# Optimization experiments

Measured on AMD Instinct MI355X. Metric: run time of the kernel, lower is better.

The kernel has to match this reference:

```python
import jax, jax.numpy as jnp
import numpy as np

B, T, D_IN = 64, 365, 10
D_MODEL, N_HEAD, D_K = 256, 16, 8
D_HEAD = D_MODEL // N_HEAD  # 16, value head dim
MAX_POS = 365 + 2 * 30      # max_position + 2*max_temporal_shift = 425
BN_EPS = 1e-5


def _pos_table(n_pos, d, temp=1000.0):
    # standard sinusoidal table (frozen in the original via Embedding.from_pretrained)
    pos = np.arange(n_pos)[:, None].astype(np.float64)
    i = np.arange(d)[None, :]
    angle = pos / np.power(temp, 2 * (i // 2) / d)
    tab = np.where(i % 2 == 0, np.sin(angle), np.cos(angle))
    return jnp.asarray(tab, jnp.float32)

POS_TABLE = _pos_table(MAX_POS, D_MODEL)


def _linear_layer(x, W, b, g, beta):
    # LinearLayer = Linear -> BatchNorm1d (train-mode batch stats, per-feature) -> ReLU
    y = x @ W.T + b
    ax = tuple(range(y.ndim - 1))
    mu = y.mean(ax, keepdims=True)
    var = y.var(ax, keepdims=True)  # biased var, matches torch BN
    y = (y - mu) * jax.lax.rsqrt(var + BN_EPS) * g + beta
    return jax.nn.relu(y)


def _forward(positions, x, w1, b1, g1, e1, w2, b2, g2, e2, w3, b3, g3, e3,
             ws1, ws2, wi, bi, gi, ei, wk, bk, wq, bq, wm, bm, gm, em,
             wd1, bd1, gd1, ed1, wd2, bd2, gd2, ed2, wc, bc):
    # channel MLP encoder: 10 -> 64 -> 128 -> 256
    out = _linear_layer(x, w1, b1, g1, e1)
    out = _linear_layer(out, w2, b2, g2, e2)
    out = _linear_layer(out, w3, b3, g3, e3)                    # [B,T,256]
    # channel SE attention: avgpool over time, 2 linears (no bias), sigmoid, residual
    pooled = out.mean(axis=1, keepdims=True)                     # [B,1,256]
    att = jax.nn.sigmoid(jax.nn.relu(pooled @ ws1.T) @ ws2.T)    # [B,1,256]
    out = att * pooled + out                                     # broadcast residual
    # temporal attention block
    h = _linear_layer(out, wi, bi, gi, ei)                       # inconv -> [B,T,256]
    e = h + POS_TABLE[positions]                                 # add positional encoding
    q = (e @ wq.T + bq).reshape(B, T, N_HEAD, D_K)
    k = (e @ wk.T + bk).reshape(B, T, N_HEAD, D_K)
    v = e.reshape(B, T, N_HEAD, D_HEAD)
    # 'cross' attention: full score matrix, mean over key dim, softmax over query dim
    scores = jnp.einsum('bthd,bshd->bhts', q, k) / jnp.sqrt(jnp.float32(D_K))  # [B,H,T,T]
    scores = scores.mean(axis=-1)                                # [B,H,T]
    a = jax.nn.softmax(scores, axis=-1)                          # [B,H,T]
    y = jnp.einsum('bht,bthe->bhe', a, v).reshape(B, D_MODEL)    # [B,256]
    y = _linear_layer(y, wm, bm, gm, em)                         # mlp 256 -> 128
    # decoder: 128 -> 64 -> 32 -> num_classes
    z = _linear_layer(y, wd1, bd1, gd1, ed1)
    z = _linear_layer(z, wd2, bd2, gd2, ed2)
    return z @ wc.T + bc                                         # logits [B,10]


def setup_inputs():
    key = jax.random.key(0)
    ks = jax.random.split(key, 16)
    n = lambda i, sh: jax.random.normal(ks[i], sh, jnp.float32) * 0.05
    z, o = jnp.zeros, jnp.ones
    return {
        'x': jax.random.normal(ks[0], (B, T, D_IN), jnp.float32),
        'positions': jnp.sort(jax.random.randint(ks[1], (B, T), 0, MAX_POS), axis=-1),
        'w1': n(2, (64, D_IN)), 'b1': z(64), 'g1': o(64), 'e1': z(64),
        'w2': n(3, (128, 64)), 'b2': z(128), 'g2': o(128), 'e2': z(128),
        'w3': n(4, (256, 128)), 'b3': z(256), 'g3': o(256), 'e3': z(256),
        'ws1': n(5, (16, 256)), 'ws2': n(6, (256, 16)),
        'wi': n(7, (256, 256)), 'bi': z(256), 'gi': o(256), 'ei': z(256),
        'wk': n(8, (128, 256)), 'bk': z(128),
        'wq': n(9, (128, 256)), 'bq': z(128),
        'wm': n(10, (128, 256)), 'bm': z(128), 'gm': o(128), 'em': z(128),
        'wd1': n(11, (64, 128)), 'bd1': z(64), 'gd1': o(64), 'ed1': z(64),
        'wd2': n(12, (32, 64)), 'bd2': z(32), 'gd2': o(32), 'ed2': z(32),
        'wc': n(13, (10, 32)), 'bc': z(10),
    }


def reference(x, positions, w1, b1, g1, e1, w2, b2, g2, e2, w3, b3, g3, e3,
              ws1, ws2, wi, bi, gi, ei, wk, bk, wq, bq, wm, bm, gm, em,
              wd1, bd1, gd1, ed1, wd2, bd2, gd2, ed2, wc, bc):
    return _forward(positions, x, w1, b1, g1, e1, w2, b2, g2, e2, w3, b3, g3, e3,
                    ws1, ws2, wi, bi, gi, ei, wk, bk, wq, bq, wm, bm, gm, em,
                    wd1, bd1, gd1, ed1, wd2, bd2, gd2, ed2, wc, bc)
```

## Files before the change

### kernel.cpp

```cpp
#include <hip/hip_runtime.h>
#include <hip/hip_bf16.h>
#include <math.h>

#define TT 365
#define BT 23360
#define NPOS 425

typedef __hip_bfloat16 bf16;
typedef __attribute__((ext_vector_type(8))) short s16x8;
typedef __attribute__((ext_vector_type(4))) float f32x4;

__device__ __forceinline__ float b2f(bf16 v) { return __bfloat162float(v); }
__device__ __forceinline__ bf16  f2b(float v) { return __float2bfloat16(v); }
__device__ __forceinline__ float u2f(unsigned u) { return __uint_as_float(u); }
__device__ __forceinline__ short f2bs(float v) { bf16 h = __float2bfloat16(v); return *reinterpret_cast<short*>(&h); }
__device__ __forceinline__ void unpack8(uint4 raw, float* v) {
    v[0] = u2f(raw.x << 16); v[1] = u2f(raw.x & 0xffff0000u);
    v[2] = u2f(raw.y << 16); v[3] = u2f(raw.y & 0xffff0000u);
    v[4] = u2f(raw.z << 16); v[5] = u2f(raw.z & 0xffff0000u);
    v[6] = u2f(raw.w << 16); v[7] = u2f(raw.w & 0xffff0000u);
}

__global__ __launch_bounds__(256) void prep_kernel(
    float* __restrict__ stats, float* __restrict__ pooled, float* __restrict__ esum,
    const float* __restrict__ w2, const float* __restrict__ w3, const float* __restrict__ wi,
    bf16* __restrict__ whi, bf16* __restrict__ wlo, float* __restrict__ tab)
{
    int i = blockIdx.x * 256 + threadIdx.x;
    if (i < 2048)  { stats[i] = 0.f; return; }  i -= 2048;
    if (i < 16384) { pooled[i] = 0.f; return; } i -= 16384;
    if (i < 16384) { esum[i] = 0.f; return; }   i -= 16384;
    if (i < 106496) {
        float w; int out, k, Kq, base;
        if (i < 8192)       { int j = i;         Kq = 64;  out = j >> 6; k = j & 63;  base = 0;     w = w2[j]; }
        else if (i < 40960) { int j = i - 8192;  Kq = 128; out = j >> 7; k = j & 127; base = 8192;  w = w3[j]; }
        else                { int j = i - 40960; Kq = 256; out = j >> 8; k = j & 255; base = 40960; w = wi[j]; }
        int P = base + ((out >> 6) * (Kq >> 3) + (k >> 3)) * 512 + (out & 63) * 8 + (k & 7);
        bf16 h = f2b(w);
        whi[P] = h;
        wlo[P] = f2b(w - b2f(h));
        return;
    } i -= 106496;
    if (i < 108800) {
        int c = i & 255, p = i >> 8;
        float e = (float)(2 * (c >> 1)) * (1.f / 256.f);
        float ang = (float)p * exp2f(-e * 9.96578428466209f);
        tab[i] = (c & 1) ? cosf(ang) : sinf(ang);
    }
}

__global__ __launch_bounds__(256) void gemm_l1_kernel(
    const float* __restrict__ x,
    const float* __restrict__ W, const float* __restrict__ bias,
    bf16* __restrict__ Y, float* __restrict__ stats)
{
    const int t  = threadIdx.x;
    const int tx = t & 15, ty = t >> 4;
    const int row0 = blockIdx.x * 64;
    __shared__ float As[64][17];
    __shared__ float Ws[16][65];
    __shared__ float red_s[4][64];
    __shared__ float red_q[4][64];
    float acc[4][4];
#pragma unroll
    for (int rr = 0; rr < 4; ++rr)
#pragma unroll
        for (int cc = 0; cc < 4; ++cc) acc[rr][cc] = 0.f;
#pragma unroll
    for (int i = 0; i < 4; ++i) {
        int idx = t + i * 256, r = idx >> 4, c = idx & 15;
        As[r][c] = (c < 10) ? x[(size_t)(row0 + r) * 10 + c] : 0.f;
    }
#pragma unroll
    for (int i = 0; i < 4; ++i) {
        int idx = t + i * 256, c = idx >> 4, kk = idx & 15;
        Ws[kk][c] = (kk < 10) ? W[(size_t)c * 10 + kk] : 0.f;
    }
    __syncthreads();
#pragma unroll
    for (int kk = 0; kk < 10; ++kk) {
        float a[4];
#pragma unroll
        for (int rr = 0; rr < 4; ++rr) a[rr] = As[ty * 4 + rr][kk];
#pragma unroll
        for (int cc = 0; cc < 4; ++cc) {
            float w = Ws[kk][cc * 16 + tx];
#pragma unroll
            for (int rr = 0; rr < 4; ++rr) acc[rr][cc] = fmaf(a[rr], w, acc[rr][cc]);
        }
    }
    float s_cc[4], q_cc[4];
#pragma unroll
    for (int cc = 0; cc < 4; ++cc) { s_cc[cc] = 0.f; q_cc[cc] = 0.f; }
#pragma unroll
    for (int rr = 0; rr < 4; ++rr) {
        int row = row0 + ty * 4 + rr;
#pragma unroll
        for (int cc = 0; cc < 4; ++cc) {
            int col = cc * 16 + tx;
            float v = acc[rr][cc] + bias[col];
            Y[(size_t)row * 64 + col] = f2b(v);
            s_cc[cc] += v; q_cc[cc] += v * v;
        }
    }
    int w = t >> 6;
#pragma unroll
    for (int cc = 0; cc < 4; ++cc) {
        float s = s_cc[cc], q = q_cc[cc];
        s += __shfl_xor(s, 16); q += __shfl_xor(q, 16);
        s += __shfl_xor(s, 32); q += __shfl_xor(q, 32);
        if ((t & 63) < 16) { red_s[w][cc * 16 + tx] = s; red_q[w][cc * 16 + tx] = q; }
    }
    __syncthreads();
    if (t < 64) {
        float s = red_s[0][t] + red_s[1][t] + red_s[2][t] + red_s[3][t];
        float q = red_q[0][t] + red_q[1][t] + red_q[2][t] + red_q[3][t];
        atomicAdd(&stats[t], s);
        atomicAdd(&stats[256 + t], q);
    }
}

template<int MODE, int K, int NCB>
__global__ __launch_bounds__(256) void mfma_gemm(
    const bf16* __restrict__ A,
    const bf16* __restrict__ Whi, const bf16* __restrict__ Wlo,
    const float* __restrict__ bias,
    bf16* __restrict__ Y, int ldY, float* __restrict__ stats,
    const float* __restrict__ bnstats, const float* __restrict__ bng,
    const float* __restrict__ bnb, const float* __restrict__ sebuf)
{
    constexpr int KC = 64;
    constexpr int VPC = (KC / 8) * 64;
    __shared__ s16x8 Wl[2][KC / 8][64];
    __shared__ float red_s[4][64];
    __shared__ float red_q[4][64];
    __shared__ float scb[MODE ? K : 1];
    __shared__ float shb[MODE ? K : 1];
    const int t = threadIdx.x, wave = t >> 6, lane = t & 63;
    const int n16 = lane & 15, quad = lane >> 4;
    constexpr int nwg = 365 * NCB;
    constexpr int sq = nwg >> 3, sr = nwg & 7;
    const int xcd = blockIdx.x & 7, sidx = blockIdx.x >> 3;
    const int L = (xcd < sr ? xcd * (sq + 1) : sr * (sq + 1) + (xcd - sr) * sq) + sidx;
    const int rowblk = L / NCB, colblk = L - rowblk * NCB;
    const int m0 = rowblk * 64 + wave * 16;
    const int col0 = colblk * 64;
    const int arow = m0 + n16;
    const bf16* Ap = A + (size_t)arow * K + quad * 8;
    s16x8 af[K / 32];
#pragma unroll
    for (int i = 0; i < K / 32; ++i) af[i] = *(const s16x8*)(Ap + i * 32);
    const s16x8* gH = (const s16x8*)Whi + (size_t)colblk * (K >> 3) * 64;
    const s16x8* gL = (const s16x8*)Wlo + (size_t)colblk * (K >> 3) * 64;
    s16x8* WlF = (s16x8*)Wl;
#pragma unroll
    for (int idx = t; idx < VPC; idx += 256) {
        WlF[idx]       = gH[idx];
        WlF[VPC + idx] = gL[idx];
    }
    if (MODE) {
        if (t < K) {
            float mu = bnstats[t] * (1.f / (float)BT);
            float var = bnstats[256 + t] * (1.f / (float)BT) - mu * mu;
            float sc = rsqrtf(var + 1e-5f) * bng[t];
            scb[t] = sc; shb[t] = bnb[t] - mu * sc;
        }
    }
    __syncthreads();
    if (MODE) {
        const float* sev = (MODE == 2) ? (sebuf + (arow / TT) * 256) : nullptr;
#pragma unroll
        for (int i = 0; i < K / 32; ++i) {
            s16x8 raw = af[i];
            int kb = i * 32 + quad * 8;
#pragma unroll
            for (int j = 0; j < 8; ++j) {
                float y = u2f(((unsigned)(unsigned short)raw[j]) << 16);
                float v = fmaxf(fmaf(y, scb[kb + j], shb[kb + j]), 0.f);
                if (MODE == 2) v += sev[kb + j];
                raw[j] = f2bs(v);
            }
            af[i] = raw;
        }
    }
    f32x4 acc[4];
    f32x4 zero = {0.f, 0.f, 0.f, 0.f};
#pragma unroll
    for (int ct = 0; ct < 4; ++ct) acc[ct] = zero;
#pragma unroll
    for (int kc = 0; kc < K; kc += KC) {
        if (kc) {
            __syncthreads();
#pragma unroll
            for (int idx = t; idx < VPC; idx += 256) {
                WlF[idx]       = gH[(kc >> 3) * 64 + idx];
                WlF[VPC + idx] = gL[(kc >> 3) * 64 + idx];
            }
            __syncthreads();
        }
#pragma unroll
        for (int i = 0; i < KC / 32; ++i) {
            const int kgq = i * 4 + quad;
            const s16x8 a = af[(kc >> 5) + i];
#pragma unroll
            for (int ct = 0; ct < 4; ++ct) {
                s16x8 bl = Wl[1][kgq][ct * 16 + n16];
                s16x8 bh = Wl[0][kgq][ct * 16 + n16];
                acc[ct] = __builtin_amdgcn_mfma_f32_16x16x32_bf16(a, bl, acc[ct], 0, 0, 0);
                acc[ct] = __builtin_amdgcn_mfma_f32_16x16x32_bf16(a, bh, acc[ct], 0, 0, 0);
            }
        }
    }
#pragma unroll
    for (int ct = 0; ct < 4; ++ct) {
        int col = col0 + ct * 16 + n16;
        float bv = bias[col];
        float s = 0.f, q = 0.f;
#pragma unroll
        for (int r = 0; r < 4; ++r) {
            float v = acc[ct][r] + bv;
            int row = m0 + quad * 4 + r;
            Y[(size_t)row * ldY + col] = f2b(v);
            s += v; q += v * v;
        }
        s += __shfl_xor(s, 16); q += __shfl_xor(q, 16);
        s += __shfl_xor(s, 32); q += __shfl_xor(q, 32);
        if (quad == 0) { red_s[wave][ct * 16 + n16] = s; red_q[wave][ct * 16 + n16] = q; }
    }
    if (stats) {
        __syncthreads();
        if (t < 64) {
            float s = red_s[0][t] + red_s[1][t] + red_s[2][t] + red_s[3][t];
            float q = red_q[0][t] + red_q[1][t] + red_q[2][t] + red_q[3][t];
            atomicAdd(&stats[col0 + t], s);
            atomicAdd(&stats[256 + col0 + t], q);
        }
    }
}

__global__ __launch_bounds__(256) void pool_partial_kernel(
    const bf16* __restrict__ Y3, const float* __restrict__ stats,
    const float* __restrict__ g3, const float* __restrict__ e3,
    float* __restrict__ pooled)
{
    const int b = blockIdx.x, part = blockIdx.y, t = threadIdx.x;
    const int cg = t & 31, rs = t >> 5;
    __shared__ float scb[256], shb[256];
    __shared__ float pp[8][256];
    {
        float mu = stats[t] * (1.f / (float)BT);
        float var = stats[256 + t] * (1.f / (float)BT) - mu * mu;
        float sc = rsqrtf(var + 1e-5f) * g3[t];
        scb[t] = sc; shb[t] = e3[t] - mu * sc;
    }
    __syncthreads();
    float acc[8] = {0.f,0.f,0.f,0.f,0.f,0.f,0.f,0.f};
    const int r0 = part * 46;
#pragma unroll
    for (int i = 0; i < 6; ++i) {
        int l = rs + i * 8;
        int r = r0 + l;
        if (l < 46 && r < TT) {
            uint4 raw = *(const uint4*)(Y3 + ((size_t)b * TT + r) * 256 + cg * 8);
            float v[8];
            unpack8(raw, v);
#pragma unroll
            for (int j = 0; j < 8; ++j)
                acc[j] += fmaxf(fmaf(v[j], scb[cg * 8 + j], shb[cg * 8 + j]), 0.f);
        }
    }
#pragma unroll
    for (int j = 0; j < 8; ++j) pp[rs][cg * 8 + j] = acc[j];
    __syncthreads();
    float s = 0.f;
#pragma unroll
    for (int r = 0; r < 8; ++r) s += pp[r][t];
    atomicAdd(&pooled[b * 256 + t], s);
}

__global__ __launch_bounds__(256) void se_mlp_kernel(const float* __restrict__ pooled,
                                                     const float* __restrict__ ws1,
                                                     const float* __restrict__ ws2,
                                                     float* __restrict__ se) {
    int b = blockIdx.x, f = threadIdx.x;
    __shared__ float pl[256];
    __shared__ float hidden[16];
    float p = pooled[b * 256 + f] * (1.f / (float)TT);
    pl[f] = p;
    __syncthreads();
    if (f < 16) {
        float h = 0.f;
        for (int k2 = 0; k2 < 256; ++k2) h = fmaf(pl[k2], ws1[f * 256 + k2], h);
        hidden[f] = fmaxf(h, 0.f);
    }
    __syncthreads();
    float a = 0.f;
    for (int k2 = 0; k2 < 16; ++k2) a = fmaf(hidden[k2], ws2[f * 16 + k2], a);
    a = 1.f / (1.f + expf(-a));
    se[b * 256 + f] = a * p;
}

__global__ __launch_bounds__(256) void bnrelu8_kernel(
    const bf16* __restrict__ Y, const float* __restrict__ stats,
    const float* __restrict__ g, const float* __restrict__ beta,
    bf16* __restrict__ Out, const float* __restrict__ tab, const int* __restrict__ pos,
    float* __restrict__ esum) {
    __shared__ float pe[8][256];
    const int t = threadIdx.x;
    int i = (blockIdx.x * 256 + t) * 8;
    int col = i & 255, row = i >> 8;
    uint4 raw = *(const uint4*)(Y + i);
    float v[8];
    unpack8(raw, v);
    const float invM = 1.f / (float)BT;
    const float* tr = tab + pos[row] * 256 + col;
    bf16 tmp[8] __attribute__((aligned(16)));
    float* pr = &pe[t >> 5][col];
#pragma unroll
    for (int j = 0; j < 8; ++j) {
        float mu  = stats[col + j] * invM;
        float var = stats[256 + col + j] * invM - mu * mu;
        float o = (v[j] - mu) * rsqrtf(var + 1e-5f) * g[col + j] + beta[col + j];
        float ev = fmaxf(o, 0.f) + tr[j];
        tmp[j] = f2b(ev);
        pr[j] = ev;
    }
    *(uint4*)(Out + i) = *(const uint4*)tmp;
    __syncthreads();
    const int g0 = blockIdx.x * 8;
    const int b0 = g0 / TT, b1 = (g0 + 7) / TT;
    const int split = (b1 != b0) ? (b1 * TT - g0) : 8;
    float s0 = 0.f, s1 = 0.f;
#pragma unroll
    for (int rr = 0; rr < 8; ++rr) {
        float vv = pe[rr][t];
        if (rr < split) s0 += vv; else s1 += vv;
    }
    atomicAdd(&esum[b0 * 256 + t], s0);
    if (b1 != b0) atomicAdd(&esum[b1 * 256 + t], s1);
}

__global__ __launch_bounds__(64) void attn3_kernel(
    const bf16* __restrict__ e, const float* __restrict__ esum,
    const float* __restrict__ wk, const float* __restrict__ bk,
    const float* __restrict__ wq, const float* __restrict__ bq,
    float* __restrict__ yv)
{
    __shared__ float kqL[256];
    __shared__ float aw[368];
    const int b = blockIdx.x, h = blockIdx.y;
    const int lane = threadIdx.x;
    float4 es = *(const float4*)(esum + b * 256 + lane * 4);
    float ks[8];
#pragma unroll
    for (int d = 0; d < 8; ++d) {
        float4 wv = *(const float4*)(wk + (size_t)(h * 8 + d) * 256 + lane * 4);
        ks[d] = es.x * wv.x + es.y * wv.y + es.z * wv.z + es.w * wv.w;
    }
#pragma unroll
    for (int off = 1; off < 64; off <<= 1)
#pragma unroll
        for (int d = 0; d < 8; ++d) ks[d] += __shfl_xor(ks[d], off);
#pragma unroll
    for (int d = 0; d < 8; ++d) ks[d] += (float)TT * bk[h * 8 + d];
    {
        float4 kq = {0.f, 0.f, 0.f, 0.f};
#pragma unroll
        for (int d = 0; d < 8; ++d) {
            float4 wv = *(const float4*)(wq + (size_t)(h * 8 + d) * 256 + lane * 4);
            kq.x = fmaf(ks[d], wv.x, kq.x);
            kq.y = fmaf(ks[d], wv.y, kq.y);
            kq.z = fmaf(ks[d], wv.z, kq.z);
            kq.w = fmaf(ks[d], wv.w, kq.w);
        }
        *(float4*)&kqL[lane * 4] = kq;
    }
    float cb = 0.f;
#pragma unroll
    for (int d = 0; d < 8; ++d) cb = fmaf(ks[d], bq[h * 8 + d], cb);
    __syncthreads();
    const int gp = lane >> 3, gl = lane & 7;
    float4 kr[8];
    {
        const float4* kq4 = (const float4*)(kqL + gl * 32);
#pragma unroll
        for (int u = 0; u < 8; ++u) kr[u] = kq4[u];
    }
    const float scale = 1.f / (sqrtf(8.f) * (float)TT);
    const bf16* ebs = e + (size_t)b * TT * 256 + gl * 32;
    for (int it = 0; it < 46; ++it) {
        int r = it * 8 + gp;
        if (r < TT) {
            const bf16* ep = ebs + (size_t)r * 256;
            float dot = 0.f;
#pragma unroll
            for (int u = 0; u < 4; ++u) {
                uint4 raw = *(const uint4*)(ep + u * 8);
                float v[8];
                unpack8(raw, v);
                float4 ka = kr[u * 2], kb2 = kr[u * 2 + 1];
                dot += v[0] * ka.x + v[1] * ka.y + v[2] * ka.z + v[3] * ka.w
                     + v[4] * kb2.x + v[5] * kb2.y + v[6] * kb2.z + v[7] * kb2.w;
            }
            dot += __shfl_xor(dot, 1);
            dot += __shfl_xor(dot, 2);
            dot += __shfl_xor(dot, 4);
            if (gl == 0) aw[r] = (dot + cb) * scale;
        }
    }
    __syncthreads();
    float sv[6];
    float m = -1e30f;
#pragma unroll
    for (int i = 0; i < 6; ++i) {
        int r = lane + i * 64;
        sv[i] = (r < TT) ? aw[r] : -1e30f;
        m = fmaxf(m, sv[i]);
    }
#pragma unroll
    for (int off = 1; off < 64; off <<= 1) m = fmaxf(m, __shfl_xor(m, off));
    float sum = 0.f;
#pragma unroll
    for (int i = 0; i < 6; ++i) {
        float ev = (sv[i] > -1e29f) ? expf(sv[i] - m) : 0.f;
        sv[i] = ev; sum += ev;
    }
#pragma unroll
    for (int off = 1; off < 64; off <<= 1) sum += __shfl_xor(sum, off);
    float inv = 1.f / sum;
#pragma unroll
    for (int i = 0; i < 6; ++i) {
        int r = lane + i * 64;
        if (r < TT) aw[r] = sv[i] * inv;
    }
    __syncthreads();
    const int half = lane & 1, rs = lane >> 1;
    float acc[8] = {0.f,0.f,0.f,0.f,0.f,0.f,0.f,0.f};
    const bf16* ebase = e + (size_t)b * TT * 256 + h * 16 + half * 8;
#pragma unroll
    for (int i = 0; i < 12; ++i) {
        int r = rs + i * 32;
        if (r < TT) {
            uint4 raw = *(const uint4*)(ebase + (size_t)r * 256);
            float v[8];
            unpack8(raw, v);
            float a = aw[r];
#pragma unroll
            for (int j = 0; j < 8; ++j) acc[j] = fmaf(a, v[j], acc[j]);
        }
    }
#pragma unroll
    for (int off = 2; off < 64; off <<= 1)
#pragma unroll
        for (int j = 0; j < 8; ++j) acc[j] += __shfl_xor(acc[j], off);
    if (lane < 2) {
        float* op = yv + b * 256 + h * 16 + half * 8;
#pragma unroll
        for (int j = 0; j < 8; ++j) op[j] = acc[j];
    }
}


__global__ __launch_bounds__(256) void tail_m_kernel(
    const float* __restrict__ yv, const float* __restrict__ wm,
    const float* __restrict__ gm, const float* __restrict__ em,
    float* __restrict__ z1)
{
    __shared__ float Xq[4160];
    const int t = threadIdx.x, r = t & 63, cw = t >> 6;
    const int c0 = blockIdx.x * 8 + cw * 2;
    const float4* wf4 = (const float4*)wm;
    float acc[2] = {0.f, 0.f};
    for (int p = 0; p < 4; ++p) {
        if (p) __syncthreads();
        for (int i = t; i < 4096; i += 256) {
            int kk = i & 63, rr = i >> 6;
            Xq[kk * 65 + rr] = yv[rr * 256 + p * 64 + kk];
        }
        __syncthreads();
#pragma unroll 4
        for (int k4 = 0; k4 < 16; ++k4) {
            float xv[4];
#pragma unroll
            for (int j = 0; j < 4; ++j) xv[j] = Xq[(k4 * 4 + j) * 65 + r];
#pragma unroll
            for (int c = 0; c < 2; ++c) {
                float4 w = wf4[(c0 + c) * 64 + p * 16 + k4];
                acc[c] = fmaf(xv[0], w.x, acc[c]);
                acc[c] = fmaf(xv[1], w.y, acc[c]);
                acc[c] = fmaf(xv[2], w.z, acc[c]);
                acc[c] = fmaf(xv[3], w.w, acc[c]);
            }
        }
    }
#pragma unroll
    for (int c = 0; c < 2; ++c) {
        float v = acc[c];
        float s = v, q = v * v;
#pragma unroll
        for (int off = 1; off < 64; off <<= 1) { s += __shfl_xor(s, off); q += __shfl_xor(q, off); }
        float mu = s * (1.f / 64.f), var = q * (1.f / 64.f) - mu * mu;
        float sc = rsqrtf(var + 1e-5f) * gm[c0 + c], sh = em[c0 + c] - mu * sc;
        z1[r * 128 + c0 + c] = fmaxf(fmaf(v, sc, sh), 0.f);
    }
}

__global__ __launch_bounds__(256) void tail_d1_kernel(
    const float* __restrict__ z1, const float* __restrict__ wd1,
    const float* __restrict__ gd1, const float* __restrict__ ed1,
    float* __restrict__ z2)
{
    __shared__ float Xq[4160];
    const int t = threadIdx.x, r = t & 63, cw = t >> 6;
    const int c0 = blockIdx.x * 8 + cw * 2;
    const float4* wf4 = (const float4*)wd1;
    float acc[2] = {0.f, 0.f};
    for (int p = 0; p < 2; ++p) {
        if (p) __syncthreads();
        for (int i = t; i < 4096; i += 256) {
            int kk = i & 63, rr = i >> 6;
            Xq[kk * 65 + rr] = z1[rr * 128 + p * 64 + kk];
        }
        __syncthreads();
#pragma unroll 4
        for (int k4 = 0; k4 < 16; ++k4) {
            float xv[4];
#pragma unroll
            for (int j = 0; j < 4; ++j) xv[j] = Xq[(k4 * 4 + j) * 65 + r];
#pragma unroll
            for (int c = 0; c < 2; ++c) {
                float4 w = wf4[(c0 + c) * 32 + p * 16 + k4];
                acc[c] = fmaf(xv[0], w.x, acc[c]);
                acc[c] = fmaf(xv[1], w.y, acc[c]);
                acc[c] = fmaf(xv[2], w.z, acc[c]);
                acc[c] = fmaf(xv[3], w.w, acc[c]);
            }
        }
    }
#pragma unroll
    for (int c = 0; c < 2; ++c) {
        float v = acc[c];
        float s = v, q = v * v;
#pragma unroll
        for (int off = 1; off < 64; off <<= 1) { s += __shfl_xor(s, off); q += __shfl_xor(q, off); }
        float mu = s * (1.f / 64.f), var = q * (1.f / 64.f) - mu * mu;
        float sc = rsqrtf(var + 1e-5f) * gd1[c0 + c], sh = ed1[c0 + c] - mu * sc;
        z2[r * 64 + c0 + c] = fmaxf(fmaf(v, sc, sh), 0.f);
    }
}

__global__ __launch_bounds__(256) void tail_d2c_kernel(
    const float* __restrict__ z2, const float* __restrict__ wd2,
    const float* __restrict__ gd2, const float* __restrict__ ed2,
    const float* __restrict__ wc, const float* __restrict__ bc,
    float* __restrict__ out)
{
    __shared__ float Xq[4160];
    __shared__ float Z3t[2048];
    __shared__ float WcL[320];
    const int t = threadIdx.x, r = t & 63, cw = t >> 6;
    const int c03 = cw * 8;
    for (int i = t; i < 4096; i += 256) {
        int kk = i & 63, rr = i >> 6;
        Xq[kk * 65 + rr] = z2[rr * 64 + kk];
    }
    if (t < 80) ((float4*)WcL)[t] = ((const float4*)wc)[t];
    __syncthreads();
    const float4* wf4 = (const float4*)wd2;
    float acc[8] = {0.f,0.f,0.f,0.f,0.f,0.f,0.f,0.f};
#pragma unroll 4
    for (int k4 = 0; k4 < 16; ++k4) {
        float xv[4];
#pragma unroll
        for (int j = 0; j < 4; ++j) xv[j] = Xq[(k4 * 4 + j) * 65 + r];
#pragma unroll
        for (int c = 0; c < 8; ++c) {
            float4 w = wf4[(c03 + c) * 16 + k4];
            acc[c] = fmaf(xv[0], w.x, acc[c]);
            acc[c] = fmaf(xv[1], w.y, acc[c]);
            acc[c] = fmaf(xv[2], w.z, acc[c]);
            acc[c] = fmaf(xv[3], w.w, acc[c]);
        }
    }
#pragma unroll
    for (int c = 0; c < 8; ++c) {
        float v = acc[c];
        float s = v, q = v * v;
#pragma unroll
        for (int off = 1; off < 64; off <<= 1) { s += __shfl_xor(s, off); q += __shfl_xor(q, off); }
        float mu = s * (1.f / 64.f), var = q * (1.f / 64.f) - mu * mu;
        float sc = rsqrtf(var + 1e-5f) * gd2[c03 + c], sh = ed2[c03 + c] - mu * sc;
        Z3t[(c03 + c) * 64 + r] = fmaxf(fmaf(v, sc, sh), 0.f);
    }
    __syncthreads();
#pragma unroll
    for (int i = 0; i < 3; ++i) {
        int idx = t + i * 256;
        if (idx < 640) {
            int rr = idx / 10, c = idx - rr * 10;
            float s = bc[c];
#pragma unroll
            for (int kk = 0; kk < 32; ++kk) s = fmaf(Z3t[kk * 64 + rr], WcL[c * 32 + kk], s);
            out[idx] = s;
        }
    }
}


extern "C" void kernel_launch(void* const* d_in, const int* in_sizes, int n_in,
                              void* d_out, int out_size, void* d_ws, size_t ws_size,
                              hipStream_t stream) {
    (void)in_sizes; (void)n_in; (void)out_size; (void)ws_size;
    const float* x  = (const float*)d_in[0];
    const int* pos  = (const int*)d_in[1];
    const float *w1 = (const float*)d_in[2],  *b1 = (const float*)d_in[3],
                *g1 = (const float*)d_in[4],  *e1 = (const float*)d_in[5];
    const float *w2 = (const float*)d_in[6],  *b2 = (const float*)d_in[7],
                *g2 = (const float*)d_in[8],  *e2 = (const float*)d_in[9];
    const float *w3 = (const float*)d_in[10], *b3 = (const float*)d_in[11],
                *g3 = (const float*)d_in[12], *e3 = (const float*)d_in[13];
    const float *ws1 = (const float*)d_in[14], *ws2 = (const float*)d_in[15];
    const float *wi = (const float*)d_in[16], *bi = (const float*)d_in[17],
                *gi = (const float*)d_in[18], *ei = (const float*)d_in[19];
    const float *wk = (const float*)d_in[20], *bk = (const float*)d_in[21];
    const float *wq = (const float*)d_in[22], *bq = (const float*)d_in[23];
    const float *wm = (const float*)d_in[24], *bm = (const float*)d_in[25],
                *gm = (const float*)d_in[26], *em = (const float*)d_in[27];
    const float *wd1 = (const float*)d_in[28], *bd1 = (const float*)d_in[29],
                *gd1 = (const float*)d_in[30], *ed1 = (const float*)d_in[31];
    const float *wd2 = (const float*)d_in[32], *bd2 = (const float*)d_in[33],
                *gd2 = (const float*)d_in[34], *ed2 = (const float*)d_in[35];
    const float *wc = (const float*)d_in[36], *bc = (const float*)d_in[37];
    float* out = (float*)d_out;
    (void)bm; (void)bd1; (void)bd2;

    char* w8 = (char*)d_ws;
    bf16*  actA   = (bf16*)(w8);
    bf16*  actB   = (bf16*)(w8 + 11960320);
    bf16*  whi    = (bf16*)(w8 + 23920640);
    bf16*  wlo    = (bf16*)(w8 + 24199168);
    float* tab    = (float*)(w8 + 24477696);
    float* stats  = (float*)(w8 + 24912896);
    float* pooled = (float*)(w8 + 24921088);
    float* sebuf  = (float*)(w8 + 24986624);
    float* esum   = (float*)(w8 + 25052160);
    float* yvb    = (float*)(w8 + 25117696);
    float* z1     = esum;
    float* z2     = sebuf;

    prep_kernel<<<977, 256, 0, stream>>>(stats, pooled, esum, w2, w3, wi, whi, wlo, tab);
    gemm_l1_kernel<<<365, 256, 0, stream>>>(x, w1, b1, actB, stats);
    mfma_gemm<1, 64, 2><<<730, 256, 0, stream>>>(actB, whi, wlo, b2,
                                                 actA, 128, stats + 512, stats, g1, e1, nullptr);
    mfma_gemm<1, 128, 4><<<1460, 256, 0, stream>>>(actA, whi + 8192, wlo + 8192, b3,
                                                   actB, 256, stats + 1024, stats + 512, g2, e2, nullptr);
    pool_partial_kernel<<<dim3(64, 8), 256, 0, stream>>>(actB, stats + 1024, g3, e3, pooled);
    se_mlp_kernel<<<64, 256, 0, stream>>>(pooled, ws1, ws2, sebuf);
    mfma_gemm<2, 256, 4><<<1460, 256, 0, stream>>>(actB, whi + 40960, wlo + 40960, bi,
                                                   actA, 256, stats + 1536, stats + 1024, g3, e3, sebuf);
    bnrelu8_kernel<<<BT * 256 / 2048, 256, 0, stream>>>(actA, stats + 1536, gi, ei, actB, tab, pos, esum);
    attn3_kernel<<<dim3(64, 16), 64, 0, stream>>>(actB, esum, wk, bk, wq, bq, yvb);
    tail_m_kernel<<<16, 256, 0, stream>>>(yvb, wm, gm, em, z1);
    tail_d1_kernel<<<8, 256, 0, stream>>>(z1, wd1, gd1, ed1, z2);
    tail_d2c_kernel<<<1, 256, 0, stream>>>(z2, wd2, gd2, ed2, wc, bc, out);
}
```

Measured before the change: 291.2 us.

## Fuse SE MLP into pooling and merge tail kernels via last-block counters

Folds the SE MLP into the pooling kernel: the last of the 8 partial blocks per batch, found with an atomic counter, computes the SE attention. The three tail kernels merge into one, where the last of 16 blocks runs the d1, d2 and classifier stages serially. This removes three kernel launches and their inter-kernel gaps. In exchange, the d1 stage now runs on a single block instead of 8, and correctness depends on fence and atomic ordering.

```diff
diff --git a/kernel.cpp b/kernel.cpp
--- a/kernel.cpp
+++ b/kernel.cpp
@@ -23,6 +23,7 @@
 
 __global__ __launch_bounds__(256) void prep_kernel(
     float* __restrict__ stats, float* __restrict__ pooled, float* __restrict__ esum,
+    float* __restrict__ syncb,
     const float* __restrict__ w2, const float* __restrict__ w3, const float* __restrict__ wi,
     bf16* __restrict__ whi, bf16* __restrict__ wlo, float* __restrict__ tab)
 {
@@ -30,6 +31,7 @@
     if (i < 2048)  { stats[i] = 0.f; return; }  i -= 2048;
     if (i < 16384) { pooled[i] = 0.f; return; } i -= 16384;
     if (i < 16384) { esum[i] = 0.f; return; }   i -= 16384;
+    if (i < 256)   { syncb[i] = 0.f; return; }  i -= 256;
     if (i < 106496) {
         float w; int out, k, Kq, base;
         if (i < 8192)       { int j = i;         Kq = 64;  out = j >> 6; k = j & 63;  base = 0;     w = w2[j]; }
@@ -238,15 +240,19 @@
     }
 }
 
-__global__ __launch_bounds__(256) void pool_partial_kernel(
+__global__ __launch_bounds__(256) void pool_se_kernel(
     const bf16* __restrict__ Y3, const float* __restrict__ stats,
     const float* __restrict__ g3, const float* __restrict__ e3,
-    float* __restrict__ pooled)
+    float* __restrict__ pooled,
+    const float* __restrict__ ws1, const float* __restrict__ ws2,
+    int* __restrict__ cntB, float* __restrict__ se)
 {
     const int b = blockIdx.x, part = blockIdx.y, t = threadIdx.x;
     const int cg = t & 31, rs = t >> 5;
     __shared__ float scb[256], shb[256];
     __shared__ float pp[8][256];
+    __shared__ float hid[16];
+    __shared__ int lf;
     {
         float mu = stats[t] * (1.f / (float)BT);
         float var = stats[256 + t] * (1.f / (float)BT) - mu * mu;
@@ -276,28 +282,27 @@
 #pragma unroll
     for (int r = 0; r < 8; ++r) s += pp[r][t];
     atomicAdd(&pooled[b * 256 + t], s);
-}
-
-__global__ __launch_bounds__(256) void se_mlp_kernel(const float* __restrict__ pooled,
-                                                     const float* __restrict__ ws1,
-                                                     const float* __restrict__ ws2,
-                                                     float* __restrict__ se) {
-    int b = blockIdx.x, f = threadIdx.x;
-    __shared__ float pl[256];
-    __shared__ float hidden[16];
-    float p = pooled[b * 256 + f] * (1.f / (float)TT);
-    pl[f] = p;
-    __syncthreads();
-    if (f < 16) {
+    if (t == 0) {
+        int v = __hip_atomic_fetch_add(&cntB[b], 1, __ATOMIC_ACQ_REL, __HIP_MEMORY_SCOPE_AGENT);
+        lf = (v == 7) ? 1 : 0;
+    }
+    __syncthreads();
+    if (!lf) return;
+    float p = __hip_atomic_load(&pooled[b * 256 + t], __ATOMIC_RELAXED, __HIP_MEMORY_SCOPE_AGENT)
+              * (1.f / (float)TT);
+    scb[t] = p;
+    __syncthreads();
+    if (t < 16) {
         float h = 0.f;
-        for (int k2 = 0; k2 < 256; ++k2) h = fmaf(pl[k2], ws1[f * 256 + k2], h);
-        hidden[f] = fmaxf(h, 0.f);
+        for (int k2 = 0; k2 < 256; ++k2) h = fmaf(scb[k2], ws1[t * 256 + k2], h);
+        hid[t] = fmaxf(h, 0.f);
     }
     __syncthreads();
     float a = 0.f;
-    for (int k2 = 0; k2 < 16; ++k2) a = fmaf(hidden[k2], ws2[f * 16 + k2], a);
+#pragma unroll
+    for (int k2 = 0; k2 < 16; ++k2) a = fmaf(hid[k2], ws2[t * 16 + k2], a);
     a = 1.f / (1.f + expf(-a));
-    se[b * 256 + f] = a * p;
+    se[b * 256 + t] = a * p;
 }
 
 __global__ __launch_bounds__(256) void bnrelu8_kernel(
@@ -460,148 +465,145 @@
     }
 }
 
-
-__global__ __launch_bounds__(256) void tail_m_kernel(
+__global__ __launch_bounds__(256) void tail_fused_kernel(
     const float* __restrict__ yv, const float* __restrict__ wm,
     const float* __restrict__ gm, const float* __restrict__ em,
-    float* __restrict__ z1)
+    const float* __restrict__ wd1, const float* __restrict__ gd1, const float* __restrict__ ed1,
+    const float* __restrict__ wd2, const float* __restrict__ gd2, const float* __restrict__ ed2,
+    const float* __restrict__ wc, const float* __restrict__ bc,
+    float* __restrict__ z1, int* __restrict__ tcnt, float* __restrict__ out)
 {
-    __shared__ float Xq[4160];
+    __shared__ float Lb[14864];
+    __shared__ int lf;
     const int t = threadIdx.x, r = t & 63, cw = t >> 6;
-    const int c0 = blockIdx.x * 8 + cw * 2;
-    const float4* wf4 = (const float4*)wm;
-    float acc[2] = {0.f, 0.f};
-    for (int p = 0; p < 4; ++p) {
-        if (p) __syncthreads();
-        for (int i = t; i < 4096; i += 256) {
-            int kk = i & 63, rr = i >> 6;
-            Xq[kk * 65 + rr] = yv[rr * 256 + p * 64 + kk];
+    {
+        float* Xq = Lb;
+        const int c0 = blockIdx.x * 8 + cw * 2;
+        const float4* wf4 = (const float4*)wm;
+        float acc[2] = {0.f, 0.f};
+        for (int p = 0; p < 4; ++p) {
+            if (p) __syncthreads();
+            for (int i = t; i < 4096; i += 256) {
+                int kk = i & 63, rr = i >> 6;
+                Xq[kk * 65 + rr] = yv[rr * 256 + p * 64 + kk];
+            }
+            __syncthreads();
+#pragma unroll 4
+            for (int k4 = 0; k4 < 16; ++k4) {
+                float xv[4];
+#pragma unroll
+                for (int j = 0; j < 4; ++j) xv[j] = Xq[(k4 * 4 + j) * 65 + r];
+#pragma unroll
+                for (int c = 0; c < 2; ++c) {
+                    float4 w = wf4[(c0 + c) * 64 + p * 16 + k4];
+                    acc[c] = fmaf(xv[0], w.x, acc[c]);
+                    acc[c] = fmaf(xv[1], w.y, acc[c]);
+                    acc[c] = fmaf(xv[2], w.z, acc[c]);
+                    acc[c] = fmaf(xv[3], w.w, acc[c]);
+                }
+            }
+        }
+#pragma unroll
+        for (int c = 0; c < 2; ++c) {
+            float v = acc[c];
+            float s = v, q = v * v;
+#pragma unroll
+            for (int off = 1; off < 64; off <<= 1) { s += __shfl_xor(s, off); q += __shfl_xor(q, off); }
+            float mu = s * (1.f / 64.f), var = q * (1.f / 64.f) - mu * mu;
+            float sc = rsqrtf(var + 1e-5f) * gm[c0 + c], sh = em[c0 + c] - mu * sc;
+            z1[r * 128 + c0 + c] = fmaxf(fmaf(v, sc, sh), 0.f);
+        }
+    }
+    __threadfence();
+    if (t == 0) {
+        int v = __hip_atomic_fetch_add(tcnt, 1, __ATOMIC_ACQ_REL, __HIP_MEMORY_SCOPE_AGENT);
+        lf = (v == 15) ? 1 : 0;
+    }
+    __syncthreads();
+    if (!lf) return;
+    __threadfence();
+    float* Xq2 = Lb;
+    float* z2L = Lb + 8320;
+    float* Z3t = Lb + 12480;
+    float* WcL = Lb + 14528;
+    {
+        for (int i = t; i < 8192; i += 256) {
+            int c = i & 127, rr = i >> 7;
+            Xq2[c * 65 + rr] = z1[rr * 128 + c];
         }
         __syncthreads();
+        const float4* w4 = (const float4*)wd1;
+        float acc[16];
+#pragma unroll
+        for (int j = 0; j < 16; ++j) acc[j] = 0.f;
+#pragma unroll 4
+        for (int k4 = 0; k4 < 32; ++k4) {
+            float x0 = Xq2[(k4 * 4 + 0) * 65 + r];
+            float x1 = Xq2[(k4 * 4 + 1) * 65 + r];
+            float x2 = Xq2[(k4 * 4 + 2) * 65 + r];
+            float x3 = Xq2[(k4 * 4 + 3) * 65 + r];
+#pragma unroll
+            for (int j = 0; j < 16; ++j) {
+                float4 w = w4[(cw * 16 + j) * 32 + k4];
+                acc[j] = fmaf(x0, w.x, acc[j]);
+                acc[j] = fmaf(x1, w.y, acc[j]);
+                acc[j] = fmaf(x2, w.z, acc[j]);
+                acc[j] = fmaf(x3, w.w, acc[j]);
+            }
+        }
+#pragma unroll
+        for (int j = 0; j < 16; ++j) {
+            int c = cw * 16 + j;
+            float v = acc[j];
+            float s = v, q = v * v;
+#pragma unroll
+            for (int off = 1; off < 64; off <<= 1) { s += __shfl_xor(s, off); q += __shfl_xor(q, off); }
+            float mu = s * (1.f / 64.f), var = q * (1.f / 64.f) - mu * mu;
+            float sc = rsqrtf(var + 1e-5f) * gd1[c], sh = ed1[c] - mu * sc;
+            z2L[c * 65 + r] = fmaxf(fmaf(v, sc, sh), 0.f);
+        }
+        if (t < 80) ((float4*)WcL)[t] = ((const float4*)wc)[t];
+    }
+    __syncthreads();
+    {
+        const int c03 = cw * 8;
+        const float4* wf4 = (const float4*)wd2;
+        float acc[8] = {0.f,0.f,0.f,0.f,0.f,0.f,0.f,0.f};
 #pragma unroll 4
         for (int k4 = 0; k4 < 16; ++k4) {
             float xv[4];
 #pragma unroll
-            for (int j = 0; j < 4; ++j) xv[j] = Xq[(k4 * 4 + j) * 65 + r];
-#pragma unroll
-            for (int c = 0; c < 2; ++c) {
-                float4 w = wf4[(c0 + c) * 64 + p * 16 + k4];
+            for (int j = 0; j < 4; ++j) xv[j] = z2L[(k4 * 4 + j) * 65 + r];
+#pragma unroll
+            for (int c = 0; c < 8; ++c) {
+                float4 w = wf4[(c03 + c) * 16 + k4];
                 acc[c] = fmaf(xv[0], w.x, acc[c]);
                 acc[c] = fmaf(xv[1], w.y, acc[c]);
                 acc[c] = fmaf(xv[2], w.z, acc[c]);
                 acc[c] = fmaf(xv[3], w.w, acc[c]);
             }
         }
-    }
-#pragma unroll
-    for (int c = 0; c < 2; ++c) {
-        float v = acc[c];
-        float s = v, q = v * v;
-#pragma unroll
-        for (int off = 1; off < 64; off <<= 1) { s += __shfl_xor(s, off); q += __shfl_xor(q, off); }
-        float mu = s * (1.f / 64.f), var = q * (1.f / 64.f) - mu * mu;
-        float sc = rsqrtf(var + 1e-5f) * gm[c0 + c], sh = em[c0 + c] - mu * sc;
-        z1[r * 128 + c0 + c] = fmaxf(fmaf(v, sc, sh), 0.f);
-    }
-}
-
-__global__ __launch_bounds__(256) void tail_d1_kernel(
-    const float* __restrict__ z1, const float* __restrict__ wd1,
-    const float* __restrict__ gd1, const float* __restrict__ ed1,
-    float* __restrict__ z2)
-{
-    __shared__ float Xq[4160];
-    const int t = threadIdx.x, r = t & 63, cw = t >> 6;
-    const int c0 = blockIdx.x * 8 + cw * 2;
-    const float4* wf4 = (const float4*)wd1;
-    float acc[2] = {0.f, 0.f};
-    for (int p = 0; p < 2; ++p) {
-        if (p) __syncthreads();
-        for (int i = t; i < 4096; i += 256) {
-            int kk = i & 63, rr = i >> 6;
-            Xq[kk * 65 + rr] = z1[rr * 128 + p * 64 + kk];
+#pragma unroll
+        for (int c = 0; c < 8; ++c) {
+            float v = acc[c];
+            float s = v, q = v * v;
+#pragma unroll
+            for (int off = 1; off < 64; off <<= 1) { s += __shfl_xor(s, off); q += __shfl_xor(q, off); }
+            float mu = s * (1.f / 64.f), var = q * (1.f / 64.f) - mu * mu;
+            float sc = rsqrtf(var + 1e-5f) * gd2[c03 + c], sh = ed2[c03 + c] - mu * sc;
+            Z3t[(c03 + c) * 64 + r] = fmaxf(fmaf(v, sc, sh), 0.f);
         }
         __syncthreads();
-#pragma unroll 4
-        for (int k4 = 0; k4 < 16; ++k4) {
-            float xv[4];
-#pragma unroll
-            for (int j = 0; j < 4; ++j) xv[j] = Xq[(k4 * 4 + j) * 65 + r];
-#pragma unroll
-            for (int c = 0; c < 2; ++c) {
-                float4 w = wf4[(c0 + c) * 32 + p * 16 + k4];
-                acc[c] = fmaf(xv[0], w.x, acc[c]);
-                acc[c] = fmaf(xv[1], w.y, acc[c]);
-                acc[c] = fmaf(xv[2], w.z, acc[c]);
-                acc[c] = fmaf(xv[3], w.w, acc[c]);
-            }
-        }
-    }
-#pragma unroll
-    for (int c = 0; c < 2; ++c) {
-        float v = acc[c];
-        float s = v, q = v * v;
-#pragma unroll
-        for (int off = 1; off < 64; off <<= 1) { s += __shfl_xor(s, off); q += __shfl_xor(q, off); }
-        float mu = s * (1.f / 64.f), var = q * (1.f / 64.f) - mu * mu;
-        float sc = rsqrtf(var + 1e-5f) * gd1[c0 + c], sh = ed1[c0 + c] - mu * sc;
-        z2[r * 64 + c0 + c] = fmaxf(fmaf(v, sc, sh), 0.f);
-    }
-}
-
-__global__ __launch_bounds__(256) void tail_d2c_kernel(
-    const float* __restrict__ z2, const float* __restrict__ wd2,
-    const float* __restrict__ gd2, const float* __restrict__ ed2,
-    const float* __restrict__ wc, const float* __restrict__ bc,
-    float* __restrict__ out)
-{
-    __shared__ float Xq[4160];
-    __shared__ float Z3t[2048];
-    __shared__ float WcL[320];
-    const int t = threadIdx.x, r = t & 63, cw = t >> 6;
-    const int c03 = cw * 8;
-    for (int i = t; i < 4096; i += 256) {
-        int kk = i & 63, rr = i >> 6;
-        Xq[kk * 65 + rr] = z2[rr * 64 + kk];
-    }
-    if (t < 80) ((float4*)WcL)[t] = ((const float4*)wc)[t];
-    __syncthreads();
-    const float4* wf4 = (const float4*)wd2;
-    float acc[8] = {0.f,0.f,0.f,0.f,0.f,0.f,0.f,0.f};
-#pragma unroll 4
-    for (int k4 = 0; k4 < 16; ++k4) {
-        float xv[4];
-#pragma unroll
-        for (int j = 0; j < 4; ++j) xv[j] = Xq[(k4 * 4 + j) * 65 + r];
-#pragma unroll
-        for (int c = 0; c < 8; ++c) {
-            float4 w = wf4[(c03 + c) * 16 + k4];
-            acc[c] = fmaf(xv[0], w.x, acc[c]);
-            acc[c] = fmaf(xv[1], w.y, acc[c]);
-            acc[c] = fmaf(xv[2], w.z, acc[c]);
-            acc[c] = fmaf(xv[3], w.w, acc[c]);
-        }
-    }
-#pragma unroll
-    for (int c = 0; c < 8; ++c) {
-        float v = acc[c];
-        float s = v, q = v * v;
-#pragma unroll
-        for (int off = 1; off < 64; off <<= 1) { s += __shfl_xor(s, off); q += __shfl_xor(q, off); }
-        float mu = s * (1.f / 64.f), var = q * (1.f / 64.f) - mu * mu;
-        float sc = rsqrtf(var + 1e-5f) * gd2[c03 + c], sh = ed2[c03 + c] - mu * sc;
-        Z3t[(c03 + c) * 64 + r] = fmaxf(fmaf(v, sc, sh), 0.f);
-    }
-    __syncthreads();
-#pragma unroll
-    for (int i = 0; i < 3; ++i) {
-        int idx = t + i * 256;
-        if (idx < 640) {
-            int rr = idx / 10, c = idx - rr * 10;
-            float s = bc[c];
-#pragma unroll
-            for (int kk = 0; kk < 32; ++kk) s = fmaf(Z3t[kk * 64 + rr], WcL[c * 32 + kk], s);
-            out[idx] = s;
+#pragma unroll
+        for (int i = 0; i < 3; ++i) {
+            int idx = t + i * 256;
+            if (idx < 640) {
+                int rr = idx / 10, c = idx - rr * 10;
+                float s = bc[c];
+#pragma unroll
+                for (int kk = 0; kk < 32; ++kk) s = fmaf(Z3t[kk * 64 + rr], WcL[c * 32 + kk], s);
+                out[idx] = s;
+            }
         }
     }
 }
@@ -645,22 +647,23 @@
     float* sebuf  = (float*)(w8 + 24986624);
     float* esum   = (float*)(w8 + 25052160);
     float* yvb    = (float*)(w8 + 25117696);
+    float* syncb  = (float*)(w8 + 25183232);
+    int*   cntB   = (int*)syncb;
+    int*   tcnt   = (int*)syncb + 64;
     float* z1     = esum;
-    float* z2     = sebuf;
-
-    prep_kernel<<<977, 256, 0, stream>>>(stats, pooled, esum, w2, w3, wi, whi, wlo, tab);
+
+    prep_kernel<<<978, 256, 0, stream>>>(stats, pooled, esum, syncb, w2, w3, wi, whi, wlo, tab);
     gemm_l1_kernel<<<365, 256, 0, stream>>>(x, w1, b1, actB, stats);
     mfma_gemm<1, 64, 2><<<730, 256, 0, stream>>>(actB, whi, wlo, b2,
                                                  actA, 128, stats + 512, stats, g1, e1, nullptr);
     mfma_gemm<1, 128, 4><<<1460, 256, 0, stream>>>(actA, whi + 8192, wlo + 8192, b3,
                                                    actB, 256, stats + 1024, stats + 512, g2, e2, nullptr);
-    pool_partial_kernel<<<dim3(64, 8), 256, 0, stream>>>(actB, stats + 1024, g3, e3, pooled);
-    se_mlp_kernel<<<64, 256, 0, stream>>>(pooled, ws1, ws2, sebuf);
+    pool_se_kernel<<<dim3(64, 8), 256, 0, stream>>>(actB, stats + 1024, g3, e3, pooled,
+                                                    ws1, ws2, cntB, sebuf);
     mfma_gemm<2, 256, 4><<<1460, 256, 0, stream>>>(actB, whi + 40960, wlo + 40960, bi,
                                                    actA, 256, stats + 1536, stats + 1024, g3, e3, sebuf);
     bnrelu8_kernel<<<BT * 256 / 2048, 256, 0, stream>>>(actA, stats + 1536, gi, ei, actB, tab, pos, esum);
     attn3_kernel<<<dim3(64, 16), 64, 0, stream>>>(actB, esum, wk, bk, wq, bq, yvb);
-    tail_m_kernel<<<16, 256, 0, stream>>>(yvb, wm, gm, em, z1);
-    tail_d1_kernel<<<8, 256, 0, stream>>>(z1, wd1, gd1, ed1, z2);
-    tail_d2c_kernel<<<1, 256, 0, stream>>>(z2, wd2, gd2, ed2, wc, bc, out);
-}
+    tail_fused_kernel<<<16, 256, 0, stream>>>(yvb, wm, gm, em, wd1, gd1, ed1,
+                                              wd2, gd2, ed2, wc, bc, z1, tcnt, out);
+}
```

After: 310.1 us. +6.5%, slower.
